# Kernel optimization log

Hardware: AMD Instinct MI355X
Metric: run time of the kernel (lower is better)

## Reference

```python
import jax, jax.numpy as jnp
import numpy as np

H = 8          # nheads
D_OUT = 1024   # tf_out_dim
D_HEAD = D_OUT // H
LN_EPS = 1e-5


def setup_inputs() -> dict:
    key = jax.random.key(0)
    ks = jax.random.split(key, 8)
    n_tok, d_in = 512, 1024
    return {
        "x": jax.random.normal(ks[0], (n_tok, d_in), jnp.float32),
        "c": jax.random.normal(ks[1], (H, n_tok, D_HEAD, D_HEAD), jnp.float32),
        "m_prev": jax.random.normal(ks[2], (H, n_tok, 1), jnp.float32),
        "n_prev": jax.random.normal(ks[3], (H, n_tok, D_HEAD), jnp.float32),
        "Wqkvo": jax.random.normal(ks[4], (d_in, 4 * D_OUT), jnp.float32) * 0.02,
        "bqkvo": jax.random.normal(ks[5], (4 * D_OUT,), jnp.float32) * 0.02,
        "Wuf": jax.random.normal(ks[6], (d_in, 2 * H), jnp.float32) * 0.02,
        "buf": jax.random.normal(ks[7], (2 * H,), jnp.float32) * 0.02,
    }


def reference(x, c, m_prev, n_prev, Wqkvo, bqkvo, Wuf, buf):
    n_tok = x.shape[0]
    scale = jnp.sqrt(jnp.float32(D_HEAD))  # sqrt(tf_out_dim / nheads)

    # projections: 'n (h d) -> h n d'
    qkvo = (x @ Wqkvo + bqkvo).reshape(n_tok, H, 4 * D_HEAD).transpose(1, 0, 2)
    q, k, v, o = jnp.split(qkvo, 4, axis=-1)          # each (H, n, d)
    k = k / scale

    # per-token outer-product update matrix ct = v k^T : (H, n, d, d)
    ct = v[..., :, None] * k[..., None, :]

    uf = (x @ Wuf + buf).reshape(n_tok, H, 2).transpose(1, 0, 2)  # (H, n, 2)
    u, f = uf[..., 0:1], uf[..., 1:2]                  # (H, n, 1)

    # stabilized exp gating (gate='exp', c is not None branch)
    m = jnp.maximum(f + m_prev, u)                     # (H, n, 1)
    ue = jnp.exp(u - m)
    fe = jnp.exp(f + m_prev - m)

    c_new = fe[..., None] * c + ue[..., None] * ct     # (H, n, d, d)
    n_new = fe * n_prev + ue * k                       # (H, n, d)

    # readout (note: original uses ct, not c_new, in the readout einsum)
    h = jnp.einsum('hnkl,hnl->hnk', ct, q)             # (H, n, d)
    nm = jnp.abs(jnp.einsum('hnk,hnk->hn', n_new, q))  # (H, n)
    h = h / jnp.maximum(nm, 1.0)[..., None]
    h = h * jax.nn.sigmoid(o)

    # 'h n d -> n (h d)', residual, LayerNorm over last dim (no affine)
    h = h.transpose(1, 0, 2).reshape(n_tok, D_OUT)
    h = x + h
    mu = jnp.mean(h, axis=-1, keepdims=True)
    var = jnp.var(h, axis=-1, keepdims=True)
    h = (h - mu) / jnp.sqrt(var + LN_EPS)
    return (c_new, h)
```

## Files before the change

### kernel.cpp

```cpp
#include <hip/hip_runtime.h>
#include <hip/hip_bf16.h>
#include <math.h>

#define KSCALE 0.08838834764831845f

typedef __bf16 bf16x8 __attribute__((ext_vector_type(8)));
typedef float  f32x4  __attribute__((ext_vector_type(4)));
typedef unsigned short u16x4 __attribute__((ext_vector_type(4)));
typedef unsigned short u16x8 __attribute__((ext_vector_type(8)));

__device__ inline unsigned short f2bf(float f) {
    unsigned int u = __float_as_uint(f);
    unsigned int r = (u + 0x7FFFu + ((u >> 16) & 1u)) >> 16;
    return (unsigned short)r;
}
__device__ __forceinline__ float bf2f(unsigned short u) {
    return __uint_as_float(((unsigned int)u) << 16);
}
__device__ __forceinline__ f32x4 LD4(const float* p) {
    return *reinterpret_cast<const f32x4*>(p);
}
__device__ __forceinline__ f32x4 LD4H(const unsigned short* p) {
    u16x4 t = *reinterpret_cast<const u16x4*>(p);
    f32x4 r = { bf2f(t[0]), bf2f(t[1]), bf2f(t[2]), bf2f(t[3]) };
    return r;
}
__device__ __forceinline__ void ST4(float* p, f32x4 v) {
    *reinterpret_cast<f32x4*>(p) = v;
}

__device__ __forceinline__ void gll16(const unsigned short* g, unsigned short* l) {
    __builtin_amdgcn_global_load_lds(
        (const __attribute__((address_space(1))) unsigned int*)g,
        (__attribute__((address_space(3))) unsigned int*)l,
        16, 0, 0);
}

__global__ __launch_bounds__(256) void prep_kernel(const float* __restrict__ x,
                                                   unsigned short* __restrict__ xb,
                                                   const float* __restrict__ W,
                                                   unsigned short* __restrict__ Wt,
                                                   const float* __restrict__ Wuf,
                                                   const float* __restrict__ buf,
                                                   const float* __restrict__ m_prev,
                                                   float* __restrict__ fe_ue) {
    int b = blockIdx.x;
    const int tid = threadIdx.x;
    if (b < 512) {
        int t = b * 256 + tid;
        float4 v = reinterpret_cast<const float4*>(x)[t];
        u16x4 o = { f2bf(v.x), f2bf(v.y), f2bf(v.z), f2bf(v.w) };
        reinterpret_cast<u16x4*>(xb)[t] = o;
    } else if (b < 1536) {
        __shared__ unsigned short tile[64][65];
        int bb = b - 512;
        int k0 = (bb & 15) * 64;
        int n0 = (bb >> 4) * 64;
        int r16 = tid >> 4, c4 = (tid & 15) * 4;
#pragma unroll
        for (int p = 0; p < 4; ++p) {
            int r = p * 16 + r16;
            float4 v = *reinterpret_cast<const float4*>(&W[(size_t)(k0 + r) * 4096 + n0 + c4]);
            tile[r][c4 + 0] = f2bf(v.x);
            tile[r][c4 + 1] = f2bf(v.y);
            tile[r][c4 + 2] = f2bf(v.z);
            tile[r][c4 + 3] = f2bf(v.w);
        }
        __syncthreads();
        int kc = (tid & 7) * 8, r32 = tid >> 3;
#pragma unroll
        for (int p = 0; p < 2; ++p) {
            int rr = p * 32 + r32;
            u16x8 o;
#pragma unroll
            for (int j = 0; j < 8; ++j) o[j] = tile[kc + j][rr];
            *reinterpret_cast<u16x8*>(&Wt[(size_t)(n0 + rr) * 1024 + k0 + kc]) = o;
        }
    } else {
        const int n = b - 1536;
        const int lane = tid & 63, w = tid >> 6;
        const float* xr = x + (size_t)n * 1024;
        float4 p = {0.f, 0.f, 0.f, 0.f};
#pragma unroll
        for (int i = 0; i < 16; ++i) {
            int k = lane + i * 64;
            float xv = xr[k];
            float4 wv = *reinterpret_cast<const float4*>(&Wuf[(size_t)k * 16 + 4 * w]);
            p.x += xv * wv.x; p.y += xv * wv.y; p.z += xv * wv.z; p.w += xv * wv.w;
        }
#pragma unroll
        for (int off = 32; off; off >>= 1) {
            p.x += __shfl_down(p.x, off);
            p.y += __shfl_down(p.y, off);
            p.z += __shfl_down(p.z, off);
            p.w += __shfl_down(p.w, off);
        }
        if (lane == 0) {
#pragma unroll
            for (int t = 0; t < 2; ++t) {
                int h = 2 * w + t;
                float u = (t ? p.z : p.x) + buf[4 * w + 2 * t];
                float f = (t ? p.w : p.y) + buf[4 * w + 2 * t + 1];
                float mp = m_prev[h * 512 + n];
                float m = fmaxf(f + mp, u);
                fe_ue[(h * 512 + n) * 2 + 0] = expf(f + mp - m);
                fe_ue[(h * 512 + n) * 2 + 1] = expf(u - m);
            }
        }
    }
}

__global__ __launch_bounds__(256) void gemm_qkvo(const unsigned short* __restrict__ A,
                                                 const unsigned short* __restrict__ Bt,
                                                 unsigned short* __restrict__ Cp) {
    __shared__ __align__(16) unsigned short As[2][64 * 64];
    __shared__ __align__(16) unsigned short Bs[2][64 * 64];
    const int kh = blockIdx.x >> 9;
    const int t9 = blockIdx.x & 511;
    const int bn = t9 & 63;
    const int bm = t9 >> 6;
    const int m0 = bm * 64, n0 = bn * 64;
    const size_t kb0 = (size_t)kh * 512;
    unsigned short* C = Cp + (size_t)kh * (512 * 4096);
    const int tid = threadIdx.x;
    const int lane = tid & 63, wave = tid >> 6;
    const int wr = wave >> 1, wc = wave & 1;
    f32x4 acc[2][2] = {};

    const int srow = lane >> 3;
    const int scol = (lane & 7) * 8;

#pragma unroll
    for (int c = 0; c < 2; ++c) {
        int chunk = wave * 2 + c;
        int row = chunk * 8 + srow;
        gll16(A + (size_t)(m0 + row) * 1024 + kb0 + scol, &As[0][chunk * 512]);
        gll16(Bt + (size_t)(n0 + row) * 1024 + kb0 + scol, &Bs[0][chunk * 512]);
    }
    __syncthreads();

    int cur = 0;
    for (int t = 0; t < 8; ++t) {
        if (t < 7) {
            size_t k0 = kb0 + (t + 1) * 64;
#pragma unroll
            for (int c = 0; c < 2; ++c) {
                int chunk = wave * 2 + c;
                int row = chunk * 8 + srow;
                gll16(A + (size_t)(m0 + row) * 1024 + k0 + scol, &As[cur ^ 1][chunk * 512]);
                gll16(Bt + (size_t)(n0 + row) * 1024 + k0 + scol, &Bs[cur ^ 1][chunk * 512]);
            }
        }
        const unsigned short* as = As[cur];
        const unsigned short* bs = Bs[cur];
        const int row = lane & 15;
        const int kof = (lane >> 4) * 8;
#pragma unroll
        for (int kk = 0; kk < 2; ++kk) {
            int kb = kk * 32 + kof;
            bf16x8 a0 = *reinterpret_cast<const bf16x8*>(&as[(wr * 32 + row) * 64 + kb]);
            bf16x8 a1 = *reinterpret_cast<const bf16x8*>(&as[(wr * 32 + 16 + row) * 64 + kb]);
            bf16x8 b0 = *reinterpret_cast<const bf16x8*>(&bs[(wc * 32 + row) * 64 + kb]);
            bf16x8 b1 = *reinterpret_cast<const bf16x8*>(&bs[(wc * 32 + 16 + row) * 64 + kb]);
            acc[0][0] = __builtin_amdgcn_mfma_f32_16x16x32_bf16(a0, b0, acc[0][0], 0, 0, 0);
            acc[0][1] = __builtin_amdgcn_mfma_f32_16x16x32_bf16(a0, b1, acc[0][1], 0, 0, 0);
            acc[1][0] = __builtin_amdgcn_mfma_f32_16x16x32_bf16(a1, b0, acc[1][0], 0, 0, 0);
            acc[1][1] = __builtin_amdgcn_mfma_f32_16x16x32_bf16(a1, b1, acc[1][1], 0, 0, 0);
        }
        __syncthreads();
        cur ^= 1;
    }

    unsigned short* cs = &As[0][0];
    const int cn = lane & 15, cm = (lane >> 4) * 4;
#pragma unroll
    for (int i = 0; i < 2; ++i)
#pragma unroll
        for (int j = 0; j < 2; ++j) {
            int r0 = wr * 32 + i * 16 + cm;
            int c0 = wc * 32 + j * 16 + cn;
#pragma unroll
            for (int v = 0; v < 4; ++v)
                cs[(r0 + v) * 64 + c0] = f2bf(acc[i][j][v]);
        }
    __syncthreads();
    {
        int row = tid >> 2, seg = tid & 3;
        const u16x8* src = reinterpret_cast<const u16x8*>(&cs[row * 64 + seg * 16]);
        u16x8* dst = reinterpret_cast<u16x8*>(&C[(size_t)(m0 + row) * 4096 + n0 + seg * 16]);
        dst[0] = src[0];
        dst[1] = src[1];
    }
}

__global__ __launch_bounds__(256) void mid_kernel(const unsigned short* __restrict__ qkvo,
                                                  const float* __restrict__ bias,
                                                  const float* __restrict__ x,
                                                  const float* __restrict__ n_prev,
                                                  const float* __restrict__ fe_ue,
                                                  float* __restrict__ uvk,
                                                  float* __restrict__ fe_arr,
                                                  float* __restrict__ h_out) {
    const int n = blockIdx.x;
    const int tid = threadIdx.x;
    const int g = tid >> 5, l = tid & 31;
    __shared__ float hs_s[1024];
    __shared__ float red[8];

    const unsigned short* bA = qkvo + (size_t)n * 4096 + g * 512;
    const unsigned short* bB = bA + (size_t)512 * 4096;
    const float* bs = bias + g * 512;
    const int d4 = l * 4;
    const int hn = g * 512 + n;

    f32x4 q = LD4H(bA + d4)       + LD4H(bB + d4)       + LD4(bs + d4);
    f32x4 k = (LD4H(bA + 128 + d4) + LD4H(bB + 128 + d4) + LD4(bs + 128 + d4)) * KSCALE;
    f32x4 v = LD4H(bA + 256 + d4) + LD4H(bB + 256 + d4) + LD4(bs + 256 + d4);
    f32x4 o = LD4H(bA + 384 + d4) + LD4H(bB + 384 + d4) + LD4(bs + 384 + d4);
    const float fe = fe_ue[hn * 2 + 0];
    const float ue = fe_ue[hn * 2 + 1];
    f32x4 np = LD4(n_prev + (size_t)hn * 128 + d4);
    f32x4 nn = fe * np + ue * k;

    float kq = q[0]*k[0] + q[1]*k[1] + q[2]*k[2] + q[3]*k[3];
    float nq = q[0]*nn[0] + q[1]*nn[1] + q[2]*nn[2] + q[3]*nn[3];
#pragma unroll
    for (int off = 16; off; off >>= 1) {
        kq += __shfl_down(kq, off, 32);
        nq += __shfl_down(nq, off, 32);
    }
    kq = __shfl(kq, 0, 32);
    nq = __shfl(nq, 0, 32);
    const float gs = kq / fmaxf(fabsf(nq), 1.0f);

    ST4(uvk + (size_t)hn * 256 + d4, ue * v);
    ST4(uvk + (size_t)hn * 256 + 128 + d4, k);
    if (l == 0) fe_arr[hn] = fe;

#pragma unroll
    for (int j = 0; j < 4; ++j)
        hs_s[g * 128 + d4 + j] = v[j] * gs / (1.f + expf(-o[j]));
    __syncthreads();

    f32x4 hv = *reinterpret_cast<const f32x4*>(&hs_s[tid * 4]);
    f32x4 xv = LD4(x + (size_t)n * 1024 + tid * 4);
    f32x4 s = hv + xv;
    float sum = s[0] + s[1] + s[2] + s[3];
    float sq  = s[0]*s[0] + s[1]*s[1] + s[2]*s[2] + s[3]*s[3];
#pragma unroll
    for (int off = 32; off; off >>= 1) {
        sum += __shfl_down(sum, off);
        sq  += __shfl_down(sq, off);
    }
    const int wv = tid >> 6;
    if ((tid & 63) == 0) { red[wv] = sum; red[4 + wv] = sq; }
    __syncthreads();
    sum = red[0] + red[1] + red[2] + red[3];
    sq  = red[4] + red[5] + red[6] + red[7];
    float mu = sum * (1.f / 1024.f);
    float var = sq * (1.f / 1024.f) - mu * mu;
    float inv = rsqrtf(var + 1e-5f);
    ST4(h_out + (size_t)n * 1024 + tid * 4, (s - mu) * inv);
}

__global__ __launch_bounds__(256) void stream_c(const float* __restrict__ c_in,
                                                const float* __restrict__ uvk,
                                                const float* __restrict__ fe_arr,
                                                float* __restrict__ c_out) {
    const int hn0 = blockIdx.x * 2;
    const int tid = threadIdx.x;
    __shared__ __align__(16) float kv_s[512];
    if (tid < 128)
        *reinterpret_cast<f32x4*>(&kv_s[tid * 4]) = LD4(uvk + (size_t)hn0 * 256 + tid * 4);
    const float fe0 = fe_arr[hn0];
    const float fe1 = fe_arr[hn0 + 1];
    __syncthreads();

    const int j4 = (tid & 31) * 4;
    const int i0 = tid >> 5;
    const f32x4 kk0 = *reinterpret_cast<const f32x4*>(&kv_s[128 + j4]);
    const f32x4 kk1 = *reinterpret_cast<const f32x4*>(&kv_s[384 + j4]);

    const f32x4* cin4 = reinterpret_cast<const f32x4*>(c_in + (size_t)hn0 * 16384);
    f32x4* cout4 = reinterpret_cast<f32x4*>(c_out + (size_t)hn0 * 16384);
#pragma unroll
    for (int it = 0; it < 16; ++it) {
        int e4 = tid + it * 256;
        float uvi = kv_s[i0 + it * 8];
        f32x4 cv = __builtin_nontemporal_load(&cin4[e4]);
        f32x4 ov = fe0 * cv + uvi * kk0;
        __builtin_nontemporal_store(ov, &cout4[e4]);
    }
#pragma unroll
    for (int it = 0; it < 16; ++it) {
        int e4 = 4096 + tid + it * 256;
        float uvi = kv_s[256 + i0 + it * 8];
        f32x4 cv = __builtin_nontemporal_load(&cin4[e4]);
        f32x4 ov = fe1 * cv + uvi * kk1;
        __builtin_nontemporal_store(ov, &cout4[e4]);
    }
}

extern "C" void kernel_launch(void* const* d_in, const int* in_sizes, int n_in,
                              void* d_out, int out_size, void* d_ws, size_t ws_size,
                              hipStream_t stream) {
    const float* x      = (const float*)d_in[0];
    const float* c_in   = (const float*)d_in[1];
    const float* m_prev = (const float*)d_in[2];
    const float* n_prev = (const float*)d_in[3];
    const float* Wqkvo  = (const float*)d_in[4];
    const float* bqkvo  = (const float*)d_in[5];
    const float* Wuf    = (const float*)d_in[6];
    const float* buf    = (const float*)d_in[7];
    float* out = (float*)d_out;
    char* ws = (char*)d_ws;

    unsigned short* xb   = (unsigned short*)(ws);
    unsigned short* Wt   = (unsigned short*)(ws + (1u << 20));
    unsigned short* qkvo = (unsigned short*)(ws + 9u * (1u << 20));
    float* fe_ue         = (float*)(ws + 17u * (1u << 20));
    float* fe_arr        = (float*)(ws + 17u * (1u << 20) + (1u << 16));
    float* uvk           = (float*)(ws + 18u * (1u << 20));

    prep_kernel<<<dim3(2048), dim3(256), 0, stream>>>(x, xb, Wqkvo, Wt, Wuf, buf, m_prev, fe_ue);
    gemm_qkvo  <<<dim3(1024), dim3(256), 0, stream>>>(xb, Wt, qkvo);
    mid_kernel <<<dim3(512),  dim3(256), 0, stream>>>(qkvo, bqkvo, x, n_prev, fe_ue,
                                                      uvk, fe_arr, out + 67108864ull);
    stream_c   <<<dim3(2048), dim3(256), 0, stream>>>(c_in, uvk, fe_arr, out);
}
```

Before: 128.9 us.

## Move gate projection into mid kernel and split stream_c to one head-token per block

The x@Wuf gate projection and exp gating move out of the prep kernel into mid_kernel. There, each block stages its x row in shared memory and does a block-wide reduction, which removes the fe_ue round trip and a second global read of x. stream_c now launches one block per (head, token) instead of two, doubling the grid and halving the work per block. The trade-off is that mid_kernel gains extra reductions and syncs on its critical path.

```diff
diff --git a/kernel.cpp b/kernel.cpp
--- a/kernel.cpp
+++ b/kernel.cpp
@@ -39,11 +39,7 @@
 __global__ __launch_bounds__(256) void prep_kernel(const float* __restrict__ x,
                                                    unsigned short* __restrict__ xb,
                                                    const float* __restrict__ W,
-                                                   unsigned short* __restrict__ Wt,
-                                                   const float* __restrict__ Wuf,
-                                                   const float* __restrict__ buf,
-                                                   const float* __restrict__ m_prev,
-                                                   float* __restrict__ fe_ue) {
+                                                   unsigned short* __restrict__ Wt) {
     int b = blockIdx.x;
     const int tid = threadIdx.x;
     if (b < 512) {
@@ -51,7 +47,7 @@
         float4 v = reinterpret_cast<const float4*>(x)[t];
         u16x4 o = { f2bf(v.x), f2bf(v.y), f2bf(v.z), f2bf(v.w) };
         reinterpret_cast<u16x4*>(xb)[t] = o;
-    } else if (b < 1536) {
+    } else {
         __shared__ unsigned short tile[64][65];
         int bb = b - 512;
         int k0 = (bb & 15) * 64;
@@ -75,37 +71,6 @@
 #pragma unroll
             for (int j = 0; j < 8; ++j) o[j] = tile[kc + j][rr];
             *reinterpret_cast<u16x8*>(&Wt[(size_t)(n0 + rr) * 1024 + k0 + kc]) = o;
-        }
-    } else {
-        const int n = b - 1536;
-        const int lane = tid & 63, w = tid >> 6;
-        const float* xr = x + (size_t)n * 1024;
-        float4 p = {0.f, 0.f, 0.f, 0.f};
-#pragma unroll
-        for (int i = 0; i < 16; ++i) {
-            int k = lane + i * 64;
-            float xv = xr[k];
-            float4 wv = *reinterpret_cast<const float4*>(&Wuf[(size_t)k * 16 + 4 * w]);
-            p.x += xv * wv.x; p.y += xv * wv.y; p.z += xv * wv.z; p.w += xv * wv.w;
-        }
-#pragma unroll
-        for (int off = 32; off; off >>= 1) {
-            p.x += __shfl_down(p.x, off);
-            p.y += __shfl_down(p.y, off);
-            p.z += __shfl_down(p.z, off);
-            p.w += __shfl_down(p.w, off);
-        }
-        if (lane == 0) {
-#pragma unroll
-            for (int t = 0; t < 2; ++t) {
-                int h = 2 * w + t;
-                float u = (t ? p.z : p.x) + buf[4 * w + 2 * t];
-                float f = (t ? p.w : p.y) + buf[4 * w + 2 * t + 1];
-                float mp = m_prev[h * 512 + n];
-                float m = fmaxf(f + mp, u);
-                fe_ue[(h * 512 + n) * 2 + 0] = expf(f + mp - m);
-                fe_ue[(h * 512 + n) * 2 + 1] = expf(u - m);
-            }
         }
     }
 }
@@ -197,28 +162,66 @@
                                                   const float* __restrict__ bias,
                                                   const float* __restrict__ x,
                                                   const float* __restrict__ n_prev,
-                                                  const float* __restrict__ fe_ue,
+                                                  const float* __restrict__ Wuf,
+                                                  const float* __restrict__ buf,
+                                                  const float* __restrict__ m_prev,
                                                   float* __restrict__ uvk,
                                                   float* __restrict__ fe_arr,
                                                   float* __restrict__ h_out) {
     const int n = blockIdx.x;
     const int tid = threadIdx.x;
     const int g = tid >> 5, l = tid & 31;
+    __shared__ float xs[1024];
+    __shared__ float red2[16][17];
+    __shared__ float dots[16];
+    __shared__ float fe_s[8], ue_s[8];
     __shared__ float hs_s[1024];
     __shared__ float red[8];
+
+    f32x4 xrow = LD4(x + (size_t)n * 1024 + tid * 4);
+    ST4(&xs[tid * 4], xrow);
+    __syncthreads();
+
+    {
+        const int c = tid & 15, kk = tid >> 4;
+        const float* wp = Wuf + (size_t)(kk * 64) * 16 + c;
+        const float* xp = &xs[kk * 64];
+        float p = 0.f;
+#pragma unroll 8
+        for (int j = 0; j < 64; ++j) p += xp[j] * wp[j * 16];
+        red2[kk][c] = p;
+    }
+    __syncthreads();
+    if (tid < 16) {
+        float d = 0.f;
+#pragma unroll
+        for (int kk = 0; kk < 16; ++kk) d += red2[kk][tid];
+        dots[tid] = d;
+    }
+    if (tid < 8) {
+        float u = dots[2 * tid] + buf[2 * tid];
+        float f = dots[2 * tid + 1] + buf[2 * tid + 1];
+        float mp = m_prev[tid * 512 + n];
+        float m = fmaxf(f + mp, u);
+        float fe = expf(f + mp - m);
+        fe_s[tid] = fe;
+        ue_s[tid] = expf(u - m);
+        fe_arr[tid * 512 + n] = fe;
+    }
+    __syncthreads();
 
     const unsigned short* bA = qkvo + (size_t)n * 4096 + g * 512;
     const unsigned short* bB = bA + (size_t)512 * 4096;
     const float* bs = bias + g * 512;
     const int d4 = l * 4;
     const int hn = g * 512 + n;
+    const float fe = fe_s[g];
+    const float ue = ue_s[g];
 
     f32x4 q = LD4H(bA + d4)       + LD4H(bB + d4)       + LD4(bs + d4);
     f32x4 k = (LD4H(bA + 128 + d4) + LD4H(bB + 128 + d4) + LD4(bs + 128 + d4)) * KSCALE;
     f32x4 v = LD4H(bA + 256 + d4) + LD4H(bB + 256 + d4) + LD4(bs + 256 + d4);
     f32x4 o = LD4H(bA + 384 + d4) + LD4H(bB + 384 + d4) + LD4(bs + 384 + d4);
-    const float fe = fe_ue[hn * 2 + 0];
-    const float ue = fe_ue[hn * 2 + 1];
     f32x4 np = LD4(n_prev + (size_t)hn * 128 + d4);
     f32x4 nn = fe * np + ue * k;
 
@@ -235,7 +238,6 @@
 
     ST4(uvk + (size_t)hn * 256 + d4, ue * v);
     ST4(uvk + (size_t)hn * 256 + 128 + d4, k);
-    if (l == 0) fe_arr[hn] = fe;
 
 #pragma unroll
     for (int j = 0; j < 4; ++j)
@@ -243,7 +245,7 @@
     __syncthreads();
 
     f32x4 hv = *reinterpret_cast<const f32x4*>(&hs_s[tid * 4]);
-    f32x4 xv = LD4(x + (size_t)n * 1024 + tid * 4);
+    f32x4 xv = *reinterpret_cast<const f32x4*>(&xs[tid * 4]);
     f32x4 s = hv + xv;
     float sum = s[0] + s[1] + s[2] + s[3];
     float sq  = s[0]*s[0] + s[1]*s[1] + s[2]*s[2] + s[3]*s[3];
@@ -267,36 +269,26 @@
                                                 const float* __restrict__ uvk,
                                                 const float* __restrict__ fe_arr,
                                                 float* __restrict__ c_out) {
-    const int hn0 = blockIdx.x * 2;
+    const int hn = blockIdx.x;
     const int tid = threadIdx.x;
-    __shared__ __align__(16) float kv_s[512];
-    if (tid < 128)
-        *reinterpret_cast<f32x4*>(&kv_s[tid * 4]) = LD4(uvk + (size_t)hn0 * 256 + tid * 4);
-    const float fe0 = fe_arr[hn0];
-    const float fe1 = fe_arr[hn0 + 1];
+    __shared__ __align__(16) float kv_s[256];
+    if (tid < 64)
+        *reinterpret_cast<f32x4*>(&kv_s[tid * 4]) = LD4(uvk + (size_t)hn * 256 + tid * 4);
+    const float fe = fe_arr[hn];
     __syncthreads();
 
     const int j4 = (tid & 31) * 4;
+    const f32x4 kk = *reinterpret_cast<const f32x4*>(&kv_s[128 + j4]);
     const int i0 = tid >> 5;
-    const f32x4 kk0 = *reinterpret_cast<const f32x4*>(&kv_s[128 + j4]);
-    const f32x4 kk1 = *reinterpret_cast<const f32x4*>(&kv_s[384 + j4]);
-
-    const f32x4* cin4 = reinterpret_cast<const f32x4*>(c_in + (size_t)hn0 * 16384);
-    f32x4* cout4 = reinterpret_cast<f32x4*>(c_out + (size_t)hn0 * 16384);
+
+    const f32x4* cin4 = reinterpret_cast<const f32x4*>(c_in + (size_t)hn * 16384);
+    f32x4* cout4 = reinterpret_cast<f32x4*>(c_out + (size_t)hn * 16384);
 #pragma unroll
     for (int it = 0; it < 16; ++it) {
         int e4 = tid + it * 256;
         float uvi = kv_s[i0 + it * 8];
         f32x4 cv = __builtin_nontemporal_load(&cin4[e4]);
-        f32x4 ov = fe0 * cv + uvi * kk0;
-        __builtin_nontemporal_store(ov, &cout4[e4]);
-    }
-#pragma unroll
-    for (int it = 0; it < 16; ++it) {
-        int e4 = 4096 + tid + it * 256;
-        float uvi = kv_s[256 + i0 + it * 8];
-        f32x4 cv = __builtin_nontemporal_load(&cin4[e4]);
-        f32x4 ov = fe1 * cv + uvi * kk1;
+        f32x4 ov = fe * cv + uvi * kk;
         __builtin_nontemporal_store(ov, &cout4[e4]);
     }
 }
@@ -318,13 +310,12 @@
     unsigned short* xb   = (unsigned short*)(ws);
     unsigned short* Wt   = (unsigned short*)(ws + (1u << 20));
     unsigned short* qkvo = (unsigned short*)(ws + 9u * (1u << 20));
-    float* fe_ue         = (float*)(ws + 17u * (1u << 20));
-    float* fe_arr        = (float*)(ws + 17u * (1u << 20) + (1u << 16));
+    float* fe_arr        = (float*)(ws + 17u * (1u << 20));
     float* uvk           = (float*)(ws + 18u * (1u << 20));
 
-    prep_kernel<<<dim3(2048), dim3(256), 0, stream>>>(x, xb, Wqkvo, Wt, Wuf, buf, m_prev, fe_ue);
+    prep_kernel<<<dim3(1536), dim3(256), 0, stream>>>(x, xb, Wqkvo, Wt);
     gemm_qkvo  <<<dim3(1024), dim3(256), 0, stream>>>(xb, Wt, qkvo);
-    mid_kernel <<<dim3(512),  dim3(256), 0, stream>>>(qkvo, bqkvo, x, n_prev, fe_ue,
-                                                      uvk, fe_arr, out + 67108864ull);
-    stream_c   <<<dim3(2048), dim3(256), 0, stream>>>(c_in, uvk, fe_arr, out);
-}
+    mid_kernel <<<dim3(512),  dim3(256), 0, stream>>>(qkvo, bqkvo, x, n_prev, Wuf, buf,
+                                                      m_prev, uvk, fe_arr, out + 67108864ull);
+    stream_c   <<<dim3(4096), dim3(256), 0, stream>>>(c_in, uvk, fe_arr, out);
+}
```

After: 127.7 us. Within noise of the previous version (-0.9%).

## Enlarge GEMM M-tile to 128 and compute k/v directly in stream_c

Applied to the files above, without the earlier changes.

The QKVO GEMM now uses 128x64 tiles, with each wave computing four A sub-tiles against two B sub-tiles. This halves the block count and raises data reuse per LDS load. stream_c now reconstructs k and ue*v straight from the bf16 split-K partials plus bias and handles one (h,n) slice per block. That removes the uvk/fe_arr intermediate buffers and mid_kernel's writes to them, and stream_c is launched before mid_kernel. The cost is that the partials get re-read, and the GEMM runs fewer, larger blocks (512) with more registers each.

```diff
diff --git a/kernel.cpp b/kernel.cpp
--- a/kernel.cpp
+++ b/kernel.cpp
@@ -113,44 +113,46 @@
 __global__ __launch_bounds__(256) void gemm_qkvo(const unsigned short* __restrict__ A,
                                                  const unsigned short* __restrict__ Bt,
                                                  unsigned short* __restrict__ Cp) {
-    __shared__ __align__(16) unsigned short As[2][64 * 64];
+    __shared__ __align__(16) unsigned short As[2][128 * 64];
     __shared__ __align__(16) unsigned short Bs[2][64 * 64];
-    const int kh = blockIdx.x >> 9;
-    const int t9 = blockIdx.x & 511;
-    const int bn = t9 & 63;
-    const int bm = t9 >> 6;
-    const int m0 = bm * 64, n0 = bn * 64;
+    const int kh = blockIdx.x >> 8;
+    const int t8 = blockIdx.x & 255;
+    const int bn = t8 & 63;
+    const int bm = t8 >> 6;
+    const int m0 = bm * 128, n0 = bn * 64;
     const size_t kb0 = (size_t)kh * 512;
     unsigned short* C = Cp + (size_t)kh * (512 * 4096);
     const int tid = threadIdx.x;
     const int lane = tid & 63, wave = tid >> 6;
     const int wr = wave >> 1, wc = wave & 1;
-    f32x4 acc[2][2] = {};
+    f32x4 acc[4][2] = {};
 
     const int srow = lane >> 3;
     const int scol = (lane & 7) * 8;
 
-#pragma unroll
-    for (int c = 0; c < 2; ++c) {
-        int chunk = wave * 2 + c;
-        int row = chunk * 8 + srow;
-        gll16(A + (size_t)(m0 + row) * 1024 + kb0 + scol, &As[0][chunk * 512]);
-        gll16(Bt + (size_t)(n0 + row) * 1024 + kb0 + scol, &Bs[0][chunk * 512]);
-    }
+#define STAGE(bufi, kofs)                                                          \
+    {                                                                              \
+        _Pragma("unroll")                                                          \
+        for (int c = 0; c < 6; ++c) {                                              \
+            int chunk = wave * 6 + c;                                              \
+            if (chunk < 16) {                                                      \
+                int row = chunk * 8 + srow;                                        \
+                gll16(A + (size_t)(m0 + row) * 1024 + (kofs) + scol,               \
+                      &As[bufi][chunk * 512]);                                     \
+            } else {                                                               \
+                int row = (chunk - 16) * 8 + srow;                                 \
+                gll16(Bt + (size_t)(n0 + row) * 1024 + (kofs) + scol,              \
+                      &Bs[bufi][(chunk - 16) * 512]);                              \
+            }                                                                      \
+        }                                                                          \
+    }
+
+    STAGE(0, kb0);
     __syncthreads();
 
     int cur = 0;
     for (int t = 0; t < 8; ++t) {
-        if (t < 7) {
-            size_t k0 = kb0 + (t + 1) * 64;
-#pragma unroll
-            for (int c = 0; c < 2; ++c) {
-                int chunk = wave * 2 + c;
-                int row = chunk * 8 + srow;
-                gll16(A + (size_t)(m0 + row) * 1024 + k0 + scol, &As[cur ^ 1][chunk * 512]);
-                gll16(Bt + (size_t)(n0 + row) * 1024 + k0 + scol, &Bs[cur ^ 1][chunk * 512]);
-            }
-        }
+        if (t < 7) STAGE(cur ^ 1, kb0 + (t + 1) * 64);
         const unsigned short* as = As[cur];
         const unsigned short* bs = Bs[cur];
         const int row = lane & 15;
@@ -158,26 +160,27 @@
 #pragma unroll
         for (int kk = 0; kk < 2; ++kk) {
             int kb = kk * 32 + kof;
-            bf16x8 a0 = *reinterpret_cast<const bf16x8*>(&as[(wr * 32 + row) * 64 + kb]);
-            bf16x8 a1 = *reinterpret_cast<const bf16x8*>(&as[(wr * 32 + 16 + row) * 64 + kb]);
             bf16x8 b0 = *reinterpret_cast<const bf16x8*>(&bs[(wc * 32 + row) * 64 + kb]);
             bf16x8 b1 = *reinterpret_cast<const bf16x8*>(&bs[(wc * 32 + 16 + row) * 64 + kb]);
-            acc[0][0] = __builtin_amdgcn_mfma_f32_16x16x32_bf16(a0, b0, acc[0][0], 0, 0, 0);
-            acc[0][1] = __builtin_amdgcn_mfma_f32_16x16x32_bf16(a0, b1, acc[0][1], 0, 0, 0);
-            acc[1][0] = __builtin_amdgcn_mfma_f32_16x16x32_bf16(a1, b0, acc[1][0], 0, 0, 0);
-            acc[1][1] = __builtin_amdgcn_mfma_f32_16x16x32_bf16(a1, b1, acc[1][1], 0, 0, 0);
+#pragma unroll
+            for (int i = 0; i < 4; ++i) {
+                bf16x8 ai = *reinterpret_cast<const bf16x8*>(&as[(wr * 64 + i * 16 + row) * 64 + kb]);
+                acc[i][0] = __builtin_amdgcn_mfma_f32_16x16x32_bf16(ai, b0, acc[i][0], 0, 0, 0);
+                acc[i][1] = __builtin_amdgcn_mfma_f32_16x16x32_bf16(ai, b1, acc[i][1], 0, 0, 0);
+            }
         }
         __syncthreads();
         cur ^= 1;
     }
+#undef STAGE
 
     unsigned short* cs = &As[0][0];
     const int cn = lane & 15, cm = (lane >> 4) * 4;
 #pragma unroll
-    for (int i = 0; i < 2; ++i)
+    for (int i = 0; i < 4; ++i)
 #pragma unroll
         for (int j = 0; j < 2; ++j) {
-            int r0 = wr * 32 + i * 16 + cm;
+            int r0 = wr * 64 + i * 16 + cm;
             int c0 = wc * 32 + j * 16 + cn;
 #pragma unroll
             for (int v = 0; v < 4; ++v)
@@ -185,11 +188,50 @@
         }
     __syncthreads();
     {
-        int row = tid >> 2, seg = tid & 3;
-        const u16x8* src = reinterpret_cast<const u16x8*>(&cs[row * 64 + seg * 16]);
-        u16x8* dst = reinterpret_cast<u16x8*>(&C[(size_t)(m0 + row) * 4096 + n0 + seg * 16]);
+        int row = tid >> 1, half = tid & 1;
+        const u16x8* src = reinterpret_cast<const u16x8*>(&cs[row * 64 + half * 32]);
+        u16x8* dst = reinterpret_cast<u16x8*>(&C[(size_t)(m0 + row) * 4096 + n0 + half * 32]);
         dst[0] = src[0];
         dst[1] = src[1];
+        dst[2] = src[2];
+        dst[3] = src[3];
+    }
+}
+
+__global__ __launch_bounds__(256) void stream_c(const float* __restrict__ c_in,
+                                                const unsigned short* __restrict__ qkvo,
+                                                const float* __restrict__ bias,
+                                                const float* __restrict__ fe_ue,
+                                                float* __restrict__ c_out) {
+    const int hn = blockIdx.x;
+    const int h = hn >> 9, n = hn & 511;
+    const int tid = threadIdx.x;
+    __shared__ __align__(16) float uv_s[128], k_s[128];
+    const float fe = fe_ue[hn * 2 + 0];
+    const float ue = fe_ue[hn * 2 + 1];
+    if (tid < 128) {
+        const unsigned short* bA = qkvo + (size_t)n * 4096 + h * 512;
+        const unsigned short* bB = bA + (size_t)512 * 4096;
+        float k = (bf2f(bA[128 + tid]) + bf2f(bB[128 + tid]) + bias[h * 512 + 128 + tid]) * KSCALE;
+        float v = bf2f(bA[256 + tid]) + bf2f(bB[256 + tid]) + bias[h * 512 + 256 + tid];
+        k_s[tid] = k;
+        uv_s[tid] = ue * v;
+    }
+    __syncthreads();
+
+    const int j4 = (tid & 31) * 4;
+    const f32x4 kk = *reinterpret_cast<const f32x4*>(&k_s[j4]);
+    const int i0 = tid >> 5;
+
+    const f32x4* cin4 = reinterpret_cast<const f32x4*>(c_in + (size_t)hn * 16384);
+    f32x4* cout4 = reinterpret_cast<f32x4*>(c_out + (size_t)hn * 16384);
+#pragma unroll
+    for (int it = 0; it < 16; ++it) {
+        int e4 = tid + it * 256;
+        float uvi = uv_s[i0 + it * 8];
+        f32x4 cv = __builtin_nontemporal_load(&cin4[e4]);
+        f32x4 ov = fe * cv + uvi * kk;
+        __builtin_nontemporal_store(ov, &cout4[e4]);
     }
 }
 
@@ -198,8 +240,6 @@
                                                   const float* __restrict__ x,
                                                   const float* __restrict__ n_prev,
                                                   const float* __restrict__ fe_ue,
-                                                  float* __restrict__ uvk,
-                                                  float* __restrict__ fe_arr,
                                                   float* __restrict__ h_out) {
     const int n = blockIdx.x;
     const int tid = threadIdx.x;
@@ -212,13 +252,13 @@
     const float* bs = bias + g * 512;
     const int d4 = l * 4;
     const int hn = g * 512 + n;
+    const float fe = fe_ue[hn * 2 + 0];
+    const float ue = fe_ue[hn * 2 + 1];
 
     f32x4 q = LD4H(bA + d4)       + LD4H(bB + d4)       + LD4(bs + d4);
     f32x4 k = (LD4H(bA + 128 + d4) + LD4H(bB + 128 + d4) + LD4(bs + 128 + d4)) * KSCALE;
     f32x4 v = LD4H(bA + 256 + d4) + LD4H(bB + 256 + d4) + LD4(bs + 256 + d4);
     f32x4 o = LD4H(bA + 384 + d4) + LD4H(bB + 384 + d4) + LD4(bs + 384 + d4);
-    const float fe = fe_ue[hn * 2 + 0];
-    const float ue = fe_ue[hn * 2 + 1];
     f32x4 np = LD4(n_prev + (size_t)hn * 128 + d4);
     f32x4 nn = fe * np + ue * k;
 
@@ -232,10 +272,6 @@
     kq = __shfl(kq, 0, 32);
     nq = __shfl(nq, 0, 32);
     const float gs = kq / fmaxf(fabsf(nq), 1.0f);
-
-    ST4(uvk + (size_t)hn * 256 + d4, ue * v);
-    ST4(uvk + (size_t)hn * 256 + 128 + d4, k);
-    if (l == 0) fe_arr[hn] = fe;
 
 #pragma unroll
     for (int j = 0; j < 4; ++j)
@@ -261,44 +297,6 @@
     float var = sq * (1.f / 1024.f) - mu * mu;
     float inv = rsqrtf(var + 1e-5f);
     ST4(h_out + (size_t)n * 1024 + tid * 4, (s - mu) * inv);
-}
-
-__global__ __launch_bounds__(256) void stream_c(const float* __restrict__ c_in,
-                                                const float* __restrict__ uvk,
-                                                const float* __restrict__ fe_arr,
-                                                float* __restrict__ c_out) {
-    const int hn0 = blockIdx.x * 2;
-    const int tid = threadIdx.x;
-    __shared__ __align__(16) float kv_s[512];
-    if (tid < 128)
-        *reinterpret_cast<f32x4*>(&kv_s[tid * 4]) = LD4(uvk + (size_t)hn0 * 256 + tid * 4);
-    const float fe0 = fe_arr[hn0];
-    const float fe1 = fe_arr[hn0 + 1];
-    __syncthreads();
-
-    const int j4 = (tid & 31) * 4;
-    const int i0 = tid >> 5;
-    const f32x4 kk0 = *reinterpret_cast<const f32x4*>(&kv_s[128 + j4]);
-    const f32x4 kk1 = *reinterpret_cast<const f32x4*>(&kv_s[384 + j4]);
-
-    const f32x4* cin4 = reinterpret_cast<const f32x4*>(c_in + (size_t)hn0 * 16384);
-    f32x4* cout4 = reinterpret_cast<f32x4*>(c_out + (size_t)hn0 * 16384);
-#pragma unroll
-    for (int it = 0; it < 16; ++it) {
-        int e4 = tid + it * 256;
-        float uvi = kv_s[i0 + it * 8];
-        f32x4 cv = __builtin_nontemporal_load(&cin4[e4]);
-        f32x4 ov = fe0 * cv + uvi * kk0;
-        __builtin_nontemporal_store(ov, &cout4[e4]);
-    }
-#pragma unroll
-    for (int it = 0; it < 16; ++it) {
-        int e4 = 4096 + tid + it * 256;
-        float uvi = kv_s[256 + i0 + it * 8];
-        f32x4 cv = __builtin_nontemporal_load(&cin4[e4]);
-        f32x4 ov = fe1 * cv + uvi * kk1;
-        __builtin_nontemporal_store(ov, &cout4[e4]);
-    }
 }
 
 extern "C" void kernel_launch(void* const* d_in, const int* in_sizes, int n_in,
@@ -319,12 +317,10 @@
     unsigned short* Wt   = (unsigned short*)(ws + (1u << 20));
     unsigned short* qkvo = (unsigned short*)(ws + 9u * (1u << 20));
     float* fe_ue         = (float*)(ws + 17u * (1u << 20));
-    float* fe_arr        = (float*)(ws + 17u * (1u << 20) + (1u << 16));
-    float* uvk           = (float*)(ws + 18u * (1u << 20));
 
     prep_kernel<<<dim3(2048), dim3(256), 0, stream>>>(x, xb, Wqkvo, Wt, Wuf, buf, m_prev, fe_ue);
-    gemm_qkvo  <<<dim3(1024), dim3(256), 0, stream>>>(xb, Wt, qkvo);
+    gemm_qkvo  <<<dim3(512),  dim3(256), 0, stream>>>(xb, Wt, qkvo);
+    stream_c   <<<dim3(4096), dim3(256), 0, stream>>>(c_in, qkvo, bqkvo, fe_ue, out);
     mid_kernel <<<dim3(512),  dim3(256), 0, stream>>>(qkvo, bqkvo, x, n_prev, fe_ue,
-                                                      uvk, fe_arr, out + 67108864ull);
-    stream_c   <<<dim3(2048), dim3(256), 0, stream>>>(c_in, uvk, fe_arr, out);
-}
+                                                      out + 67108864ull);
+}
```

After: 135.2 us. 4.9% more time.
